# Kernel tuning notes

Hardware: AMD Instinct MI355X
Metric: run time of the kernel (lower is better)

The kernel has to match this reference:

```python
import jax, jax.numpy as jnp
import numpy as np
from jax.nn import gelu

L = 4        # N_layers
M = 32       # N_modes
PA = 48      # n_processor_a
PB = 48      # n_processor_b
P = PA + PB
IN_A, IN_B = 3, 3
OUT_A, OUT_B = 1, 1
HA, HB = 256, 128
K = 3        # kernel_size
S3 = 0.05


def setup_inputs() -> dict:
    key = jax.random.key(0)
    ks = jax.random.split(key, 24)
    n = lambda k, shp, s=1.0: jax.random.normal(k, shp, dtype=jnp.float32) * s
    w_sc = 0.1
    inp = {
        "u_a": n(ks[0], (1, HA, HA)),
        "x_a": n(ks[1], (2, HA, HA)),
        "u_b": n(ks[2], (1, HB, HB)),
        "x_b": n(ks[3], (2, HB, HB)),
        # 1x1 convs stored as (Cout, Cin) matrices (equinox stores (Cout,Cin,1,1); same math)
        "enc_a_w": n(ks[4], (PA, IN_A), w_sc), "enc_a_b": n(ks[5], (PA,), w_sc),
        "enc_b_w": n(ks[6], (PB, IN_B), w_sc), "enc_b_b": n(ks[7], (PB,), w_sc),
        "dec_a_w": n(ks[8], (OUT_A, PA), w_sc), "dec_a_b": n(ks[9], (OUT_A,), w_sc),
        "dec_b_w": n(ks[10], (OUT_B, PB), w_sc), "dec_b_b": n(ks[11], (OUT_B,), w_sc),
        "c1a_w": n(ks[12], (L, PA, PA), w_sc), "c1a_b": n(ks[13], (L, PA), w_sc),
        "c2a_w": n(ks[14], (L, PA, PA), w_sc), "c2a_b": n(ks[15], (L, PA), w_sc),
        "c1b_w": n(ks[16], (L, PB, PB, K, K), w_sc), "c1b_b": n(ks[17], (L, PB), w_sc),
        "c2b_w": n(ks[18], (L, PB, PB, K, K), w_sc), "c2b_b": n(ks[19], (L, PB), w_sc),
        # complex spectral weights A as real/imag float32 parts
        "A_re": n(ks[20], (L, P, P, M, M), S3),
        "A_im": n(ks[21], (L, P, P, M, M), S3),
    }
    return inp


def _conv1x1(x, w, b):
    # x: (Cin, H, W), w: (Cout, Cin)
    return jnp.einsum("oi,ihw->ohw", w, x) + b[:, None, None]


def _convk(x, w, b):
    # x: (Cin, H, W), w: (Cout, Cin, K, K), SAME padding (padding = K//2)
    y = jax.lax.conv_general_dilated(x[None], w, (1, 1), "SAME",
                                     dimension_numbers=("NCHW", "OIHW", "NCHW"))[0]
    return y + b[:, None, None]


def _rfft2_truncate(x, m):
    c = jnp.fft.rfft2(x, norm="forward")[:, :, :m]
    return jnp.roll(c, m // 2, axis=1)[:, :m]


def _irfft2_pad(c, m, s):
    c = jnp.pad(c, ((0, 0), (0, s[0] - c.shape[1]), (0, s[1] - c.shape[2])))
    c = jnp.roll(c, -m // 2, axis=1)
    return jnp.fft.irfft2(c, s=s, norm="forward")


def _spectral(ua, ub, W):
    m = W.shape[2]
    coeff = jnp.concatenate([_rfft2_truncate(ua, m), _rfft2_truncate(ub, m)], axis=0)  # (P, m, m)
    coeff = jnp.einsum("pqmn,qmn->pmn", W, coeff)
    oa = _irfft2_pad(coeff[: ua.shape[0]], m, ua.shape[1:])
    ob = _irfft2_pad(coeff[ua.shape[0]:], m, ub.shape[1:])
    return oa, ob


def reference(u_a, x_a, u_b, x_b,
              enc_a_w, enc_a_b, enc_b_w, enc_b_b,
              dec_a_w, dec_a_b, dec_b_w, dec_b_b,
              c1a_w, c1a_b, c2a_w, c2a_b,
              c1b_w, c1b_b, c2b_w, c2b_b,
              A_re, A_im):
    ua = _conv1x1(jnp.concatenate([x_a, u_a], 0), enc_a_w, enc_a_b)
    ub = _conv1x1(jnp.concatenate([x_b, u_b], 0), enc_b_w, enc_b_b)
    for i in range(A_re.shape[0]):
        Wi = (A_re[i] + 1j * A_im[i]).astype(jnp.complex64)
        ua_, ub_ = _spectral(ua, ub, Wi)
        ua = ua + gelu(_conv1x1(gelu(_conv1x1(ua_, c1a_w[i], c1a_b[i])), c2a_w[i], c2a_b[i]))
        ub = ub + gelu(_convk(gelu(_convk(ub_, c1b_w[i], c1b_b[i])), c2b_w[i], c2b_b[i]))
    out_a = _conv1x1(ua, dec_a_w, dec_a_b)
    out_b = _conv1x1(ub, dec_b_w, dec_b_b)
    return (out_a, out_b)
```

## Files before the change

### kernel.cpp

```cpp
#include <hip/hip_runtime.h>

#define HA 256
#define WA 256
#define HB 128
#define WB 128
#define PA 48
#define PB 48
#define PP 96
#define MM 32
#define NPIXA (HA*WA)
#define NPIXB (HB*WB)

typedef short bf16x8 __attribute__((ext_vector_type(8)));
typedef float f32x4 __attribute__((ext_vector_type(4)));

__device__ __forceinline__ float gelu_f(float x) {
    float z = 0.7978845608028654f * (x + 0.044715f * x * x * x);
    float e = __expf(2.0f * z);
    return x - x / (e + 1.0f);
}

__device__ __forceinline__ short f2bf(float f) {
    unsigned u = __float_as_uint(f);
    unsigned r = (u + 0x7FFFu + ((u >> 16) & 1u)) >> 16;
    return (short)r;
}

__device__ __forceinline__ unsigned pack2(float a, float b) {
    return (unsigned)(unsigned short)f2bf(a) | ((unsigned)(unsigned short)f2bf(b) << 16);
}

__global__ __launch_bounds__(256) void k_pre(
        float* tiyA, float* tixB, float* tiyB, short* T2x,
        const float* u_a, const float* x_a, const float* u_b, const float* x_b,
        const float* wa, const float* ba, const float* wb, const float* bb,
        float* UA, float* UB,
        const float* c1b_w, const float* c2b_w, short* WT,
        short* TbfA, short* TbfB,
        const float* c1a_w, const float* c2a_w, short* WcT,
        short* Ty2A, short* Ty2B,
        short* TyIA, short* TyIB, short* T2xB) {
    const float TWO_PI = 6.28318530717958647692f;
    int bid = blockIdx.x;
    if (bid < 48) {
        int t = bid * 256 + threadIdx.x;
        if (t < MM * WA) {
            int k = t / WA, x = t - k * WA;
            int m = (k * x) & (WA - 1);
            float ang = TWO_PI * (float)m / (float)WA;
            float s, c; __sincosf(ang, &s, &c);
            float wgt = (k == 0) ? 1.0f : 2.0f;
            T2x[x*64 + 2*k]   = f2bf(wgt * c);
            T2x[x*64 + 2*k+1] = f2bf(-wgt * s);
            int ky = k - 16;
            int my = (ky * x) & (HA - 1);
            float angy = TWO_PI * (float)my / (float)HA;
            float sy, cy; __sincosf(angy, &sy, &cy);
            tiyA[2*t] = cy; tiyA[2*t+1] = sy;
        } else if (t < MM * WA + MM * WB) {
            int t2 = t - MM * WA;
            int k = t2 / WB, x = t2 - k * WB;
            int m = (k * x) & (WB - 1);
            float ang = TWO_PI * (float)m / (float)WB;
            float s, c; __sincosf(ang, &s, &c);
            float wgt = (k == 0) ? 1.0f : 2.0f;
            tixB[2*t2] = wgt * c; tixB[2*t2+1] = wgt * s;
            int ky = k - 16;
            int my = (ky * x) & (HB - 1);
            float angy = TWO_PI * (float)my / (float)HB;
            float sy, cy; __sincosf(angy, &sy, &cy);
            tiyB[2*t2] = cy; tiyB[2*t2+1] = sy;
        }
    } else if (bid < 15408) {
        int eb = bid - 48;
        int o = eb / 320;
        int chunk = eb - o * 320;
        if (chunk < 256) {
            int pix = chunk * 256 + threadIdx.x;
            UA[(size_t)o*NPIXA + pix] = wa[o*3+0]*x_a[pix] + wa[o*3+1]*x_a[NPIXA+pix]
                                      + wa[o*3+2]*u_a[pix] + ba[o];
        } else {
            int pix = (chunk - 256) * 256 + threadIdx.x;
            UB[(size_t)o*NPIXB + pix] = wb[o*3+0]*x_b[pix] + wb[o*3+1]*x_b[NPIXB+pix]
                                      + wb[o*3+2]*u_b[pix] + bb[o];
        }
    } else if (bid < 16272) {
        int g = (bid - 15408) * 256 + threadIdx.x;
        if (g < 4*2*9*48*64) {
            int l  = g / 55296;
            int r1 = g - l*55296;
            int cv = r1 / 27648;
            int r2 = r1 - cv*27648;
            int tap = r2 / 3072;
            int r3 = r2 - tap*3072;
            int oc = r3 >> 6;
            int ic = r3 & 63;
            const float* src = cv ? c2b_w : c1b_w;
            float v = 0.f;
            if (ic < 48) v = src[(((size_t)l*48 + oc)*48 + ic)*9 + tap];
            WT[g] = f2bf(v);
        }
    } else if (bid < 16336) {
        int g = (bid - 16272) * 256 + threadIdx.x;
        int col = g >> 8, x = g & 255;
        int k = col >> 1, comp = col & 1;
        int m = (k * x) & (WA - 1);
        float ang = TWO_PI * (float)m / (float)WA;
        float s, c; __sincosf(ang, &s, &c);
        float sc = 1.0f / (float)(HA * WA);
        TbfA[col*WA + x] = f2bf(comp ? -s * sc : c * sc);
    } else if (bid < 16368) {
        int g = (bid - 16336) * 256 + threadIdx.x;
        int col = g >> 7, x = g & 127;
        int k = col >> 1, comp = col & 1;
        int m = (k * x) & (WB - 1);
        float ang = TWO_PI * (float)m / (float)WB;
        float s, c; __sincosf(ang, &s, &c);
        float sc = 1.0f / (float)(HB * WB);
        TbfB[col*WB + x] = f2bf(comp ? -s * sc : c * sc);
    } else if (bid < 16464) {
        int g = (bid - 16368) * 256 + threadIdx.x;
        int l  = g / 6144;
        int r  = g - l*6144;
        int cv = r / 3072;
        int r2 = r - cv*3072;
        int oc = r2 >> 6;
        int ic = r2 & 63;
        const float* src = cv ? c2a_w : c1a_w;
        float v = 0.f;
        if (ic < 48) v = src[((size_t)l*48 + oc)*48 + ic];
        WcT[g] = f2bf(v);
    } else if (bid < 16592) {
        int g = (bid - 16464) * 256 + threadIdx.x;
        int row = g >> 9, col = g & 511;
        int j = row >> 1, comp = row & 1;
        int y = col >> 1, comp2 = col & 1;
        int my = ((j - 16) * y) & (HA - 1);
        float ang = TWO_PI * (float)my / (float)HA;
        float sy, cy; __sincosf(ang, &sy, &cy);
        float v = comp == 0 ? (comp2 == 0 ? cy : sy) : (comp2 == 0 ? -sy : cy);
        Ty2A[g] = f2bf(v);
    } else if (bid < 16656) {
        int g = (bid - 16592) * 256 + threadIdx.x;
        int row = g >> 8, col = g & 255;
        int j = row >> 1, comp = row & 1;
        int y = col >> 1, comp2 = col & 1;
        int my = ((j - 16) * y) & (HB - 1);
        float ang = TWO_PI * (float)my / (float)HB;
        float sy, cy; __sincosf(ang, &sy, &cy);
        float v = comp == 0 ? (comp2 == 0 ? cy : sy) : (comp2 == 0 ? -sy : cy);
        Ty2B[g] = f2bf(v);
    } else if (bid < 16720) {
        int g = (bid - 16656) * 256 + threadIdx.x;
        int y = g >> 6, col = g & 63;
        int j = col >> 1, comp = col & 1;
        int my = ((j - 16) * y) & (HA - 1);
        float ang = TWO_PI * (float)my / (float)HA;
        float sy, cy; __sincosf(ang, &sy, &cy);
        TyIA[g] = f2bf(comp ? sy : cy);
    } else if (bid < 16752) {
        int g = (bid - 16720) * 256 + threadIdx.x;
        int y = g >> 6, col = g & 63;
        int j = col >> 1, comp = col & 1;
        int my = ((j - 16) * y) & (HB - 1);
        float ang = TWO_PI * (float)my / (float)HB;
        float sy, cy; __sincosf(ang, &sy, &cy);
        TyIB[g] = f2bf(comp ? sy : cy);
    } else {
        int g = (bid - 16752) * 256 + threadIdx.x;
        int x = g >> 6, col = g & 63;
        int k = col >> 1, comp = col & 1;
        int m = (k * x) & (WB - 1);
        float ang = TWO_PI * (float)m / (float)WB;
        float s, c; __sincosf(ang, &s, &c);
        float wgt = (k == 0) ? 1.0f : 2.0f;
        T2xB[g] = f2bf(comp ? -wgt * s : wgt * c);
    }
}

__global__ __launch_bounds__(256) void k_fwd_x(
        const float* __restrict__ UA, const float* __restrict__ UB,
        short* __restrict__ FTA, short* __restrict__ FTB,
        const short* __restrict__ TbfA, const short* __restrict__ TbfB) {
    extern __shared__ short lsb[];
    int bid = blockIdx.x;
    const float* U; short* FT; const short* T; int N, ymask, cshift;
    if (bid < 384) { U = UA; FT = FTA; T = TbfA; N = WA; ymask = 255; cshift = 8; }
    else { bid -= 384; U = UB; FT = FTB; T = TbfB; N = WB; ymask = 127; cshift = 7; }
    int r0 = bid * 32;
    int c = r0 >> cshift;
    int ybase = r0 & ymask;
    int NP = N + 8;
    int nq = N >> 2;
    const float4* src = (const float4*)(U + (size_t)r0 * N);
    for (int i = threadIdx.x; i < 32*nq; i += 256) {
        int r = i / nq, q = i - r*nq;
        float4 v = src[i];
        *(uint2*)(lsb + r*NP + q*4) = make_uint2(pack2(v.x, v.y), pack2(v.z, v.w));
    }
    __syncthreads();
    int wv = threadIdx.x >> 6, lane = threadIdx.x & 63;
    int n = lane & 15, kg = lane >> 4;
    int col = wv*16 + n;
    const short* Tc = T + (size_t)col * N;
    f32x4 acc0 = {0.f,0.f,0.f,0.f}, acc1 = {0.f,0.f,0.f,0.f};
    for (int ks = 0; ks < (N >> 5); ++ks) {
        bf16x8 bfrag = *(const bf16x8*)(Tc + ks*32 + kg*8);
        bf16x8 a0 = *(const bf16x8*)(lsb + (size_t)n*NP + ks*32 + kg*8);
        bf16x8 a1 = *(const bf16x8*)(lsb + (size_t)(16+n)*NP + ks*32 + kg*8);
        acc0 = __builtin_amdgcn_mfma_f32_16x16x32_bf16(a0, bfrag, acc0, 0, 0, 0);
        acc1 = __builtin_amdgcn_mfma_f32_16x16x32_bf16(a1, bfrag, acc1, 0, 0, 0);
    }
    __syncthreads();
    short* trb = lsb;
    #pragma unroll
    for (int r = 0; r < 4; ++r) {
        trb[col*36 + kg*4 + r]      = f2bf(acc0[r]);
        trb[col*36 + 16 + kg*4 + r] = f2bf(acc1[r]);
    }
    __syncthreads();
    int K2 = 2 * (ymask + 1);
    for (int idx = threadIdx.x; idx < 512; idx += 256) {
        int kx = idx >> 4, q = idx & 15;
        int yl = q * 2;
        unsigned lo = (unsigned)(unsigned short)trb[(2*kx+0)*36 + yl]
                    | ((unsigned)(unsigned short)trb[(2*kx+1)*36 + yl] << 16);
        unsigned hi = (unsigned)(unsigned short)trb[(2*kx+0)*36 + yl+1]
                    | ((unsigned)(unsigned short)trb[(2*kx+1)*36 + yl+1] << 16);
        *(uint2*)(FT + ((size_t)(c*32 + kx))*K2 + 2*(size_t)ybase + yl*2) = make_uint2(lo, hi);
    }
}

__global__ __launch_bounds__(256) void k_fwd_y(
        const short* __restrict__ FTA, const short* __restrict__ FTB,
        const short* __restrict__ Ty2A, const short* __restrict__ Ty2B,
        float* __restrict__ CINa, float* __restrict__ CINb) {
    __shared__ short lsb[32*264];
    int bid = blockIdx.x;
    const short* FT; const short* Ty; int K2, NP, pbase, c, h;
    if (bid < 96) { c = bid>>1; h = bid&1; FT = FTA; Ty = Ty2A; K2 = 512; NP = 264; pbase = 0; }
    else { int b2 = bid - 96; c = b2>>1; h = b2&1; FT = FTB; Ty = Ty2B; K2 = 256; NP = 136; pbase = 48; }
    float* CO = (h == 0) ? CINa : CINb;
    int hlen = K2 >> 1;
    int nchunk = hlen >> 3;
    for (int idx = threadIdx.x; idx < 32*nchunk; idx += 256) {
        int row = idx / nchunk, q = idx - row*nchunk;
        *(uint4*)(lsb + row*NP + q*8) =
            *(const uint4*)(FT + ((size_t)c*32 + row)*K2 + h*hlen + q*8);
    }
    __syncthreads();
    int w = threadIdx.x >> 6, lane = threadIdx.x & 63;
    int n = lane & 15, kg = lane >> 4;
    f32x4 acc0 = {0.f,0.f,0.f,0.f}, acc1 = {0.f,0.f,0.f,0.f};
    int nks = hlen >> 5;
    for (int ks = 0; ks < nks; ++ks) {
        bf16x8 af = *(const bf16x8*)(Ty + (size_t)(w*16 + n)*K2 + h*hlen + ks*32 + kg*8);
        bf16x8 b0 = *(const bf16x8*)(lsb + n*NP + ks*32 + kg*8);
        bf16x8 b1 = *(const bf16x8*)(lsb + (16+n)*NP + ks*32 + kg*8);
        acc0 = __builtin_amdgcn_mfma_f32_16x16x32_bf16(af, b0, acc0, 0, 0, 0);
        acc1 = __builtin_amdgcn_mfma_f32_16x16x32_bf16(af, b1, acc1, 0, 0, 0);
    }
    #pragma unroll
    for (int r = 0; r < 4; ++r) {
        int row = w*16 + kg*4 + r;
        int j = row >> 1, comp = row & 1;
        size_t base = (((size_t)(pbase + c))*32 + j)*32;
        CO[(base + n)*2 + comp]      = acc0[r];
        CO[(base + 16 + n)*2 + comp] = acc1[r];
    }
}

__global__ __launch_bounds__(256) void k_spectral(
        const float* __restrict__ Wre, const float* __restrict__ Wim,
        const float* __restrict__ CINa, const float* __restrict__ CINb,
        float2* __restrict__ PART) {
    int part = blockIdx.y;
    int t = blockIdx.x * 256 + threadIdx.x;
    int p = t >> 8;
    int m4 = (t & 255) << 2;
    int q0 = part * 12;
    const float4* wr = (const float4*)(Wre + ((size_t)p * PP + q0) * 1024 + m4);
    const float4* wi = (const float4*)(Wim + ((size_t)p * PP + q0) * 1024 + m4);
    const float4* ca = (const float4*)(CINa + (size_t)q0 * 2048 + m4*2);
    const float4* cb = (const float4*)(CINb + (size_t)q0 * 2048 + m4*2);
    float re0=0,re1=0,re2=0,re3=0, im0=0,im1=0,im2=0,im3=0;
    #pragma unroll
    for (int q = 0; q < 12; ++q) {
        float4 a = wr[q * 256];
        float4 b = wi[q * 256];
        float4 c0 = ca[q * 512];
        float4 c1 = ca[q * 512 + 1];
        float4 d0 = cb[q * 512];
        float4 d1 = cb[q * 512 + 1];
        float cr0 = c0.x + d0.x, ci0 = c0.y + d0.y;
        float cr1 = c0.z + d0.z, ci1 = c0.w + d0.w;
        float cr2 = c1.x + d1.x, ci2 = c1.y + d1.y;
        float cr3 = c1.z + d1.z, ci3 = c1.w + d1.w;
        re0 += a.x*cr0 - b.x*ci0;  im0 += a.x*ci0 + b.x*cr0;
        re1 += a.y*cr1 - b.y*ci1;  im1 += a.y*ci1 + b.y*cr1;
        re2 += a.z*cr2 - b.z*ci2;  im2 += a.z*ci2 + b.z*cr2;
        re3 += a.w*cr3 - b.w*ci3;  im3 += a.w*ci3 + b.w*cr3;
    }
    float2* po = PART + ((size_t)part * PP + p) * 1024 + m4;
    po[0] = make_float2(re0, im0);
    po[1] = make_float2(re1, im1);
    po[2] = make_float2(re2, im2);
    po[3] = make_float2(re3, im3);
}

__global__ __launch_bounds__(256) void k_invy(
        const float2* __restrict__ PART,
        const short* __restrict__ TyIA, const short* __restrict__ TyIB,
        short* __restrict__ DA, short* __restrict__ DB) {
    __shared__ short A2[64*72];
    int bid = blockIdx.x;
    int c, yh, cb; const short* Ty; short* D;
    if (bid < 96) { c = bid >> 1; yh = bid & 1; Ty = TyIA; D = DA; cb = c; }
    else { c = bid - 96 + 48; yh = 0; Ty = TyIB; D = DB; cb = c - 48; }
    for (int idx = threadIdx.x; idx < 1024; idx += 256) {
        int j = idx >> 5, kx = idx & 31;
        float re = 0.f, im = 0.f;
        const float2* pp = PART + (size_t)c*1024 + idx;
        #pragma unroll
        for (int u = 0; u < 8; ++u) {
            float2 v = pp[(size_t)u*PP*1024];
            re += v.x; im += v.y;
        }
        A2[(2*kx+0)*72 + 2*j]   = f2bf(re);
        A2[(2*kx+0)*72 + 2*j+1] = f2bf(-im);
        A2[(2*kx+1)*72 + 2*j]   = f2bf(im);
        A2[(2*kx+1)*72 + 2*j+1] = f2bf(re);
    }
    __syncthreads();
    int wv = threadIdx.x >> 6, lane = threadIdx.x & 63;
    int n = lane & 15, kg = lane >> 4;
    #pragma unroll
    for (int ntl = 0; ntl < 2; ++ntl) {
        int nt = wv*2 + ntl;
        int y = yh*128 + nt*16 + n;
        bf16x8 bf0 = *(const bf16x8*)(Ty + (size_t)y*64 + kg*8);
        bf16x8 bf1 = *(const bf16x8*)(Ty + (size_t)y*64 + 32 + kg*8);
        #pragma unroll
        for (int mt = 0; mt < 4; ++mt) {
            bf16x8 a0 = *(const bf16x8*)(A2 + (mt*16 + n)*72 + kg*8);
            bf16x8 a1 = *(const bf16x8*)(A2 + (mt*16 + n)*72 + 32 + kg*8);
            f32x4 acc = {0.f,0.f,0.f,0.f};
            acc = __builtin_amdgcn_mfma_f32_16x16x32_bf16(a0, bf0, acc, 0, 0, 0);
            acc = __builtin_amdgcn_mfma_f32_16x16x32_bf16(a1, bf1, acc, 0, 0, 0);
            int row0 = mt*16 + kg*4;
            *(uint2*)(D + (size_t)y*3072 + cb*64 + row0) =
                make_uint2(pack2(acc[0], acc[1]), pack2(acc[2], acc[3]));
        }
    }
}

__global__ __launch_bounds__(256) void k_inv(
        const short* __restrict__ DA, const short* __restrict__ DB,
        float* __restrict__ UA, short* __restrict__ SBbf,
        const short* __restrict__ T2x, const short* __restrict__ T2xB,
        const short* __restrict__ W1T, const short* __restrict__ W2T,
        const float* __restrict__ b1v, const float* __restrict__ b2v) {
    __shared__ __attribute__((aligned(16))) char smc[37888];
    int t = threadIdx.x;
    int wv = t >> 6, lane = t & 63;
    int n = lane & 15, kg = lane >> 4;
    if (blockIdx.x < 512) {
        short* b0bf  = (short*)smc;
        short* slbf  = (short*)(smc + 18432);
        float* bl1   = (float*)(smc + 37120);
        float* bl2   = (float*)(smc + 37312);
        int y  = blockIdx.x >> 1;
        int xh = (blockIdx.x & 1) << 7;
        if (t >= 64 && t < 112) bl1[t-64] = b1v[t-64];
        if (t >= 128 && t < 176) bl2[t-128] = b2v[t-128];
        const short* DAy = DA + (size_t)y*3072;
        {
            f32x4 acc[2][3];
            #pragma unroll
            for (int i = 0; i < 2; ++i)
                #pragma unroll
                for (int mt = 0; mt < 3; ++mt)
                    acc[i][mt] = (f32x4){0.f,0.f,0.f,0.f};
            #pragma unroll
            for (int ks = 0; ks < 2; ++ks) {
                bf16x8 bfr[2];
                #pragma unroll
                for (int i = 0; i < 2; ++i) {
                    int px = xh + (wv*2 + i)*16 + n;
                    bfr[i] = *(const bf16x8*)(T2x + (size_t)px*64 + ks*32 + kg*8);
                }
                #pragma unroll
                for (int mt = 0; mt < 3; ++mt) {
                    bf16x8 af = *(const bf16x8*)(DAy + (mt*16 + n)*64 + ks*32 + kg*8);
                    #pragma unroll
                    for (int i = 0; i < 2; ++i)
                        acc[i][mt] = __builtin_amdgcn_mfma_f32_16x16x32_bf16(af, bfr[i], acc[i][mt], 0, 0, 0);
                }
            }
            #pragma unroll
            for (int i = 0; i < 2; ++i) {
                int xl = (wv*2 + i)*16 + n;
                #pragma unroll
                for (int mt = 0; mt < 3; ++mt)
                    #pragma unroll
                    for (int r = 0; r < 4; ++r)
                        slbf[xl*72 + mt*16 + kg*4 + r] = f2bf(acc[i][mt][r]);
            }
            for (int idx = t; idx < 2048; idx += 256)
                slbf[(idx >> 4)*72 + 48 + (idx & 15)] = 0;
        }
        __syncthreads();
        {
            bf16x8 aw[3][2];
            #pragma unroll
            for (int mt = 0; mt < 3; ++mt)
                #pragma unroll
                for (int ks = 0; ks < 2; ++ks)
                    aw[mt][ks] = *(const bf16x8*)(W1T + (size_t)(mt*16 + n)*64 + ks*32 + kg*8);
            f32x4 acc[2][3];
            #pragma unroll
            for (int nt = 0; nt < 2; ++nt)
                #pragma unroll
                for (int mt = 0; mt < 3; ++mt)
                    acc[nt][mt] = (f32x4){0.f,0.f,0.f,0.f};
            #pragma unroll
            for (int nt = 0; nt < 2; ++nt) {
                int ntile = wv*2 + nt;
                #pragma unroll
                for (int ks = 0; ks < 2; ++ks) {
                    bf16x8 bfrag = *(const bf16x8*)(slbf + (size_t)(ntile*16 + n)*72 + ks*32 + kg*8);
                    #pragma unroll
                    for (int mt = 0; mt < 3; ++mt)
                        acc[nt][mt] = __builtin_amdgcn_mfma_f32_16x16x32_bf16(aw[mt][ks], bfrag, acc[nt][mt], 0, 0, 0);
                }
            }
            #pragma unroll
            for (int nt = 0; nt < 2; ++nt) {
                int px = (wv*2 + nt)*16 + n;
                #pragma unroll
                for (int mt = 0; mt < 3; ++mt) {
                    int oc0 = mt*16 + kg*4;
                    float g0 = gelu_f(acc[nt][mt][0] + bl1[oc0+0]);
                    float g1 = gelu_f(acc[nt][mt][1] + bl1[oc0+1]);
                    float g2 = gelu_f(acc[nt][mt][2] + bl1[oc0+2]);
                    float g3 = gelu_f(acc[nt][mt][3] + bl1[oc0+3]);
                    *(uint2*)(b0bf + (size_t)px*72 + oc0) = make_uint2(pack2(g0,g1), pack2(g2,g3));
                }
            }
            for (int idx = t; idx < 2048; idx += 256)
                b0bf[(idx >> 4)*72 + 48 + (idx & 15)] = 0;
        }
        __syncthreads();
        {
            bf16x8 aw[3][2];
            #pragma unroll
            for (int mt = 0; mt < 3; ++mt)
                #pragma unroll
                for (int ks = 0; ks < 2; ++ks)
                    aw[mt][ks] = *(const bf16x8*)(W2T + (size_t)(mt*16 + n)*64 + ks*32 + kg*8);
            f32x4 acc[2][3];
            #pragma unroll
            for (int nt = 0; nt < 2; ++nt)
                #pragma unroll
                for (int mt = 0; mt < 3; ++mt)
                    acc[nt][mt] = (f32x4){0.f,0.f,0.f,0.f};
            #pragma unroll
            for (int nt = 0; nt < 2; ++nt) {
                int ntile = wv*2 + nt;
                #pragma unroll
                for (int ks = 0; ks < 2; ++ks) {
                    bf16x8 bfrag = *(const bf16x8*)(b0bf + (size_t)(ntile*16 + n)*72 + ks*32 + kg*8);
                    #pragma unroll
                    for (int mt = 0; mt < 3; ++mt)
                        acc[nt][mt] = __builtin_amdgcn_mfma_f32_16x16x32_bf16(aw[mt][ks], bfrag, acc[nt][mt], 0, 0, 0);
                }
            }
            #pragma unroll
            for (int nt = 0; nt < 2; ++nt) {
                int px = (wv*2 + nt)*16 + n;
                #pragma unroll
                for (int mt = 0; mt < 3; ++mt) {
                    int oc0 = mt*16 + kg*4;
                    #pragma unroll
                    for (int r = 0; r < 4; ++r) {
                        int oc = oc0 + r;
                        size_t o = (size_t)oc*NPIXA + (size_t)y*WA + xh + px;
                        UA[o] = gelu_f(acc[nt][mt][r] + bl2[oc]) + UA[o];
                    }
                }
            }
        }
    } else {
        int y = blockIdx.x - 512;
        short* sbuf = (short*)smc;
        const short* DBy = DB + (size_t)y*3072;
        #pragma unroll
        for (int ntl = 0; ntl < 2; ++ntl) {
            int nt = wv*2 + ntl;
            int x = nt*16 + n;
            bf16x8 bf0 = *(const bf16x8*)(T2xB + (size_t)x*64 + kg*8);
            bf16x8 bf1 = *(const bf16x8*)(T2xB + (size_t)x*64 + 32 + kg*8);
            #pragma unroll
            for (int mt = 0; mt < 3; ++mt) {
                bf16x8 a0 = *(const bf16x8*)(DBy + (mt*16 + n)*64 + kg*8);
                bf16x8 a1 = *(const bf16x8*)(DBy + (mt*16 + n)*64 + 32 + kg*8);
                f32x4 acc = {0.f,0.f,0.f,0.f};
                acc = __builtin_amdgcn_mfma_f32_16x16x32_bf16(a0, bf0, acc, 0, 0, 0);
                acc = __builtin_amdgcn_mfma_f32_16x16x32_bf16(a1, bf1, acc, 0, 0, 0);
                int c0 = mt*16 + kg*4;
                #pragma unroll
                for (int r = 0; r < 4; ++r)
                    sbuf[(c0 + r)*132 + x] = f2bf(acc[r]);
            }
        }
        __syncthreads();
        for (int idx = t; idx < 768; idx += 256) {
            int cc = idx >> 4, q = idx & 15;
            uint4 v = *(const uint4*)(sbuf + cc*132 + q*8);
            *(uint4*)(SBbf + (size_t)cc*NPIXB + (size_t)y*WB + q*8) = v;
        }
    }
}

__global__ __launch_bounds__(256) void k_conv3x3_mfma(
        const short* __restrict__ in, float* __restrict__ outf,
        short* __restrict__ outbf,
        const short* __restrict__ wt, const float* __restrict__ bias,
        const float* resid) {
    __shared__ float smf[3072];
    short* tile = (short*)smf;
    int y  = blockIdx.x >> 3;
    int x0 = (blockIdx.x & 7) << 4;
    int tid = threadIdx.x;

    for (int idx = tid; idx < 3456; idx += 256) {
        int r = idx / 1152;
        int rem = idx - r*1152;
        int ic = rem / 18;
        int px = rem - ic*18;
        int gy = y - 1 + r, gx = x0 - 1 + px;
        short v = 0;
        if (ic < 48 && gy >= 0 && gy < HB && gx >= 0 && gx < WB)
            v = in[(size_t)ic*NPIXB + gy*WB + gx];
        tile[(r*18 + px)*72 + ic] = v;
    }
    __syncthreads();

    int w = tid >> 6, lane = tid & 63;
    int n = lane & 15, kg = lane >> 4, m = lane & 15;
    f32x4 acc0 = {0.f,0.f,0.f,0.f}, acc1 = {0.f,0.f,0.f,0.f}, acc2 = {0.f,0.f,0.f,0.f};
    for (int s = w; s < 18; s += 4) {
        int tap = s >> 1;
        int kb = (s & 1) << 5;
        int dy = tap / 3, dx = tap - dy*3;
        bf16x8 bfrag = *(const bf16x8*)(tile + ((dy*18 + n + dx)*72 + kb + kg*8));
        const short* ap = wt + ((size_t)tap*48)*64 + kb + kg*8;
        bf16x8 a0 = *(const bf16x8*)(ap + (size_t)(m     )*64);
        bf16x8 a1 = *(const bf16x8*)(ap + (size_t)(16 + m)*64);
        bf16x8 a2 = *(const bf16x8*)(ap + (size_t)(32 + m)*64);
        acc0 = __builtin_amdgcn_mfma_f32_16x16x32_bf16(a0, bfrag, acc0, 0, 0, 0);
        acc1 = __builtin_amdgcn_mfma_f32_16x16x32_bf16(a1, bfrag, acc1, 0, 0, 0);
        acc2 = __builtin_amdgcn_mfma_f32_16x16x32_bf16(a2, bfrag, acc2, 0, 0, 0);
    }
    __syncthreads();
    float4* red = (float4*)smf;
    red[(w*3 + 0)*64 + lane] = make_float4(acc0[0], acc0[1], acc0[2], acc0[3]);
    red[(w*3 + 1)*64 + lane] = make_float4(acc1[0], acc1[1], acc1[2], acc1[3]);
    red[(w*3 + 2)*64 + lane] = make_float4(acc2[0], acc2[1], acc2[2], acc2[3]);
    __syncthreads();
    if (tid < 192) {
        int mt = tid >> 6, ln = tid & 63;
        float4 s0 = red[(0*3 + mt)*64 + ln];
        float4 s1 = red[(1*3 + mt)*64 + ln];
        float4 s2 = red[(2*3 + mt)*64 + ln];
        float4 s3 = red[(3*3 + mt)*64 + ln];
        float sum[4];
        sum[0] = s0.x + s1.x + s2.x + s3.x;
        sum[1] = s0.y + s1.y + s2.y + s3.y;
        sum[2] = s0.z + s1.z + s2.z + s3.z;
        sum[3] = s0.w + s1.w + s2.w + s3.w;
        int px = x0 + (ln & 15);
        #pragma unroll
        for (int r = 0; r < 4; ++r) {
            int oc = mt*16 + (ln >> 4)*4 + r;
            float v = sum[r] + bias[oc];
            v = gelu_f(v);
            size_t o = (size_t)oc*NPIXB + (size_t)y*WB + px;
            if (outbf) {
                outbf[o] = f2bf(v);
            } else {
                if (resid) v += resid[o];
                outf[o] = v;
            }
        }
    }
}

__global__ __launch_bounds__(256) void k_decode(
        const float* __restrict__ UA, const float* __restrict__ UB,
        const float* dwa, const float* dba,
        const float* dwb, const float* dbb, float* outp) {
    int t = blockIdx.x*256 + threadIdx.x;
    if (t < NPIXA) {
        float acc = dba[0];
        #pragma unroll 8
        for (int p = 0; p < PA; ++p) acc += dwa[p]*UA[(size_t)p*NPIXA + t];
        outp[t] = acc;
    } else {
        int u = t - NPIXA;
        float acc = dbb[0];
        #pragma unroll 8
        for (int p = 0; p < PB; ++p) acc += dwb[p]*UB[(size_t)p*NPIXB + u];
        outp[t] = acc;
    }
}

extern "C" void kernel_launch(void* const* d_in, const int* in_sizes, int n_in,
                              void* d_out, int out_size, void* d_ws, size_t ws_size,
                              hipStream_t stream) {
    const float* u_a   = (const float*)d_in[0];
    const float* x_a   = (const float*)d_in[1];
    const float* u_b   = (const float*)d_in[2];
    const float* x_b   = (const float*)d_in[3];
    const float* enc_a_w = (const float*)d_in[4];
    const float* enc_a_b = (const float*)d_in[5];
    const float* enc_b_w = (const float*)d_in[6];
    const float* enc_b_b = (const float*)d_in[7];
    const float* dec_a_w = (const float*)d_in[8];
    const float* dec_a_b = (const float*)d_in[9];
    const float* dec_b_w = (const float*)d_in[10];
    const float* dec_b_b = (const float*)d_in[11];
    const float* c1a_w = (const float*)d_in[12];
    const float* c1a_b = (const float*)d_in[13];
    const float* c2a_w = (const float*)d_in[14];
    const float* c2a_b = (const float*)d_in[15];
    const float* c1b_w = (const float*)d_in[16];
    const float* c1b_b = (const float*)d_in[17];
    const float* c2b_w = (const float*)d_in[18];
    const float* c2b_b = (const float*)d_in[19];
    const float* A_re = (const float*)d_in[20];
    const float* A_im = (const float*)d_in[21];

    float* ws = (float*)d_ws;
    size_t off = 0;
    auto alloc = [&](size_t n) { float* p = ws + off; off += n; return p; };
    short* WT    = (short*)alloc(4*2*9*48*64/2);
    short* TbfA  = (short*)alloc(64*WA/2);
    short* TbfB  = (short*)alloc(64*WB/2);
    short* WcT   = (short*)alloc(4*2*48*64/2);
    short* T2x   = (short*)alloc(WA*64/2);
    short* T2xB  = (short*)alloc(WB*64/2);
    short* Ty2A  = (short*)alloc(64*512/2);
    short* Ty2B  = (short*)alloc(64*256/2);
    short* TyIA  = (short*)alloc(HA*64/2);
    short* TyIB  = (short*)alloc(HB*64/2);
    float* TiyA  = alloc(MM*HA*2);
    float* TixB  = alloc(MM*WB*2);
    float* TiyB  = alloc(MM*HB*2);
    float* UA = alloc((size_t)PA*NPIXA);
    float* UB = alloc((size_t)PB*NPIXB);
    short* SBbf = (short*)alloc((size_t)PB*NPIXB/2);
    short* TBbf = (short*)alloc((size_t)PB*NPIXB/2);
    short* FTA = (short*)alloc((size_t)PA*MM*512/2);
    short* FTB = (short*)alloc((size_t)PB*MM*256/2);
    short* DA  = (short*)alloc((size_t)HA*3072/2);
    short* DB  = (short*)alloc((size_t)HB*3072/2);
    float* CINa = alloc((size_t)PP*MM*MM*2);
    float* CINb = alloc((size_t)PP*MM*MM*2);
    float2* PART = (float2*)alloc((size_t)8*PP*MM*MM*2);
    if (off * sizeof(float) > ws_size) return;

    k_pre<<<dim3(16784), dim3(256), 0, stream>>>(
        TiyA, TixB, TiyB, T2x,
        u_a,x_a,u_b,x_b, enc_a_w,enc_a_b,enc_b_w,enc_b_b, UA,UB,
        c1b_w, c2b_w, WT, TbfA, TbfB, c1a_w, c2a_w, WcT, Ty2A, Ty2B,
        TyIA, TyIB, T2xB);
    for (int l = 0; l < 4; ++l) {
        k_fwd_x<<<dim3(576), dim3(256), 32*(WA+8)*2, stream>>>(UA,UB,FTA,FTB,TbfA,TbfB);
        k_fwd_y<<<dim3(192), dim3(256), 0, stream>>>(FTA,FTB,Ty2A,Ty2B,CINa,CINb);
        k_spectral<<<dim3(96,8), dim3(256), 0, stream>>>(
            A_re + (size_t)l*PP*PP*MM*MM, A_im + (size_t)l*PP*PP*MM*MM,
            CINa, CINb, PART);
        k_invy<<<dim3(144), dim3(256), 0, stream>>>(PART, TyIA, TyIB, DA, DB);
        k_inv<<<dim3(512 + 128), dim3(256), 0, stream>>>(DA, DB, UA, SBbf,
            T2x, T2xB,
            WcT + (size_t)(l*2 + 0)*3072, WcT + (size_t)(l*2 + 1)*3072,
            c1a_b + (size_t)l*PA, c2a_b + (size_t)l*PA);
        k_conv3x3_mfma<<<dim3(1024), dim3(256), 0, stream>>>(SBbf, (float*)nullptr, TBbf,
            WT + (size_t)(l*2 + 0)*27648, c1b_b + (size_t)l*PB, (const float*)nullptr);
        k_conv3x3_mfma<<<dim3(1024), dim3(256), 0, stream>>>(TBbf, UB, (short*)nullptr,
            WT + (size_t)(l*2 + 1)*27648, c2b_b + (size_t)l*PB, UB);
    }
    k_decode<<<dim3(320), dim3(256), 0, stream>>>(UA, UB,
        dec_a_w, dec_a_b, dec_b_w, dec_b_b, (float*)d_out);
}
```

Before: 341.0 us.

## Switch branch-B bf16 activations to pixel-major layout and restructure 3x3 conv MFMA

The bf16 intermediates for the branch-B 3x3 convolutions are now stored pixel-major (48 channels contiguous per pixel) rather than channel-major. The conv kernel can then load its halo tile with 16-byte vector loads instead of scalar gathers. The conv kernel now covers 32 pixels per block with 6 waves, each owning one 16x16 output tile across all taps. This removes the cross-wave shared-memory reduction and its extra barriers, and the first conv writes packed bf16 pairs. In exchange the block and grid shapes change, and the channel-major fp32 output stores keep a strided pattern.

Measured after the change: 308.0 us (median of 2 runs). 1.11x faster.

```diff
diff --git a/kernel.cpp b/kernel.cpp
--- a/kernel.cpp
+++ b/kernel.cpp
@@ -514,84 +514,71 @@
             }
         }
         __syncthreads();
-        for (int idx = t; idx < 768; idx += 256) {
-            int cc = idx >> 4, q = idx & 15;
-            uint4 v = *(const uint4*)(sbuf + cc*132 + q*8);
-            *(uint4*)(SBbf + (size_t)cc*NPIXB + (size_t)y*WB + q*8) = v;
-        }
-    }
-}
-
-__global__ __launch_bounds__(256) void k_conv3x3_mfma(
+        for (int idx = t; idx < 3072; idx += 256) {
+            int x = idx / 24, cu = idx - x*24;
+            unsigned v = (unsigned)(unsigned short)sbuf[(2*cu)*132 + x]
+                       | ((unsigned)(unsigned short)sbuf[(2*cu+1)*132 + x] << 16);
+            *(unsigned*)(SBbf + ((size_t)y*WB + x)*48 + 2*cu) = v;
+        }
+    }
+}
+
+__global__ __launch_bounds__(384) void k_conv3x3_mfma(
         const short* __restrict__ in, float* __restrict__ outf,
         short* __restrict__ outbf,
         const short* __restrict__ wt, const float* __restrict__ bias,
         const float* resid) {
-    __shared__ float smf[3072];
-    short* tile = (short*)smf;
-    int y  = blockIdx.x >> 3;
-    int x0 = (blockIdx.x & 7) << 4;
+    __shared__ __attribute__((aligned(16))) short tile[3*34*72];
+    int y  = blockIdx.x >> 2;
+    int x0 = (blockIdx.x & 3) << 5;
     int tid = threadIdx.x;
-
-    for (int idx = tid; idx < 3456; idx += 256) {
-        int r = idx / 1152;
-        int rem = idx - r*1152;
-        int ic = rem / 18;
-        int px = rem - ic*18;
+    for (int idx = tid; idx < 102*6; idx += 384) {
+        int pix = idx / 6, chunk = idx - pix*6;
+        int r = pix / 34, px = pix - r*34;
         int gy = y - 1 + r, gx = x0 - 1 + px;
-        short v = 0;
-        if (ic < 48 && gy >= 0 && gy < HB && gx >= 0 && gx < WB)
-            v = in[(size_t)ic*NPIXB + gy*WB + gx];
-        tile[(r*18 + px)*72 + ic] = v;
+        uint4 v = {0u,0u,0u,0u};
+        if (gy >= 0 && gy < HB && gx >= 0 && gx < WB)
+            v = *(const uint4*)(in + ((size_t)gy*WB + gx)*48 + chunk*8);
+        *(uint4*)(tile + pix*72 + chunk*8) = v;
+    }
+    for (int idx = tid; idx < 102*2; idx += 384) {
+        int pix = idx >> 1, h = idx & 1;
+        *(uint4*)(tile + pix*72 + 48 + h*8) = (uint4){0u,0u,0u,0u};
     }
     __syncthreads();
 
-    int w = tid >> 6, lane = tid & 63;
-    int n = lane & 15, kg = lane >> 4, m = lane & 15;
-    f32x4 acc0 = {0.f,0.f,0.f,0.f}, acc1 = {0.f,0.f,0.f,0.f}, acc2 = {0.f,0.f,0.f,0.f};
-    for (int s = w; s < 18; s += 4) {
-        int tap = s >> 1;
-        int kb = (s & 1) << 5;
+    int wv = tid / 64, lane = tid & 63;
+    int n = lane & 15, kg = lane >> 4;
+    int nt = wv & 1, mt = wv >> 1;
+    f32x4 acc = {0.f,0.f,0.f,0.f};
+    #pragma unroll
+    for (int tap = 0; tap < 9; ++tap) {
         int dy = tap / 3, dx = tap - dy*3;
-        bf16x8 bfrag = *(const bf16x8*)(tile + ((dy*18 + n + dx)*72 + kb + kg*8));
-        const short* ap = wt + ((size_t)tap*48)*64 + kb + kg*8;
-        bf16x8 a0 = *(const bf16x8*)(ap + (size_t)(m     )*64);
-        bf16x8 a1 = *(const bf16x8*)(ap + (size_t)(16 + m)*64);
-        bf16x8 a2 = *(const bf16x8*)(ap + (size_t)(32 + m)*64);
-        acc0 = __builtin_amdgcn_mfma_f32_16x16x32_bf16(a0, bfrag, acc0, 0, 0, 0);
-        acc1 = __builtin_amdgcn_mfma_f32_16x16x32_bf16(a1, bfrag, acc1, 0, 0, 0);
-        acc2 = __builtin_amdgcn_mfma_f32_16x16x32_bf16(a2, bfrag, acc2, 0, 0, 0);
-    }
-    __syncthreads();
-    float4* red = (float4*)smf;
-    red[(w*3 + 0)*64 + lane] = make_float4(acc0[0], acc0[1], acc0[2], acc0[3]);
-    red[(w*3 + 1)*64 + lane] = make_float4(acc1[0], acc1[1], acc1[2], acc1[3]);
-    red[(w*3 + 2)*64 + lane] = make_float4(acc2[0], acc2[1], acc2[2], acc2[3]);
-    __syncthreads();
-    if (tid < 192) {
-        int mt = tid >> 6, ln = tid & 63;
-        float4 s0 = red[(0*3 + mt)*64 + ln];
-        float4 s1 = red[(1*3 + mt)*64 + ln];
-        float4 s2 = red[(2*3 + mt)*64 + ln];
-        float4 s3 = red[(3*3 + mt)*64 + ln];
-        float sum[4];
-        sum[0] = s0.x + s1.x + s2.x + s3.x;
-        sum[1] = s0.y + s1.y + s2.y + s3.y;
-        sum[2] = s0.z + s1.z + s2.z + s3.z;
-        sum[3] = s0.w + s1.w + s2.w + s3.w;
-        int px = x0 + (ln & 15);
+        int pxl = nt*16 + n + dx;
+        const short* brow = tile + (dy*34 + pxl)*72;
+        const short* ap = wt + (size_t)tap*3072 + (size_t)(mt*16 + n)*64;
+        #pragma unroll
+        for (int ks = 0; ks < 2; ++ks) {
+            bf16x8 bfrag = *(const bf16x8*)(brow + ks*32 + kg*8);
+            bf16x8 afrag = *(const bf16x8*)(ap + ks*32 + kg*8);
+            acc = __builtin_amdgcn_mfma_f32_16x16x32_bf16(afrag, bfrag, acc, 0, 0, 0);
+        }
+    }
+    int px_g = x0 + nt*16 + n;
+    int oc0 = mt*16 + kg*4;
+    float g0 = gelu_f(acc[0] + bias[oc0+0]);
+    float g1 = gelu_f(acc[1] + bias[oc0+1]);
+    float g2 = gelu_f(acc[2] + bias[oc0+2]);
+    float g3 = gelu_f(acc[3] + bias[oc0+3]);
+    if (outbf) {
+        *(uint2*)(outbf + ((size_t)y*WB + px_g)*48 + oc0) =
+            make_uint2(pack2(g0, g1), pack2(g2, g3));
+    } else {
+        float gv[4] = {g0, g1, g2, g3};
         #pragma unroll
         for (int r = 0; r < 4; ++r) {
-            int oc = mt*16 + (ln >> 4)*4 + r;
-            float v = sum[r] + bias[oc];
-            v = gelu_f(v);
-            size_t o = (size_t)oc*NPIXB + (size_t)y*WB + px;
-            if (outbf) {
-                outbf[o] = f2bf(v);
-            } else {
-                if (resid) v += resid[o];
-                outf[o] = v;
-            }
+            size_t o = (size_t)(oc0 + r)*NPIXB + (size_t)y*WB + px_g;
+            outf[o] = gv[r] + resid[o];
         }
     }
 }
@@ -686,9 +673,9 @@
             T2x, T2xB,
             WcT + (size_t)(l*2 + 0)*3072, WcT + (size_t)(l*2 + 1)*3072,
             c1a_b + (size_t)l*PA, c2a_b + (size_t)l*PA);
-        k_conv3x3_mfma<<<dim3(1024), dim3(256), 0, stream>>>(SBbf, (float*)nullptr, TBbf,
+        k_conv3x3_mfma<<<dim3(512), dim3(384), 0, stream>>>(SBbf, (float*)nullptr, TBbf,
             WT + (size_t)(l*2 + 0)*27648, c1b_b + (size_t)l*PB, (const float*)nullptr);
-        k_conv3x3_mfma<<<dim3(1024), dim3(256), 0, stream>>>(TBbf, UB, (short*)nullptr,
+        k_conv3x3_mfma<<<dim3(512), dim3(384), 0, stream>>>(TBbf, UB, (short*)nullptr,
             WT + (size_t)(l*2 + 1)*27648, c2b_b + (size_t)l*PB, UB);
     }
     k_decode<<<dim3(320), dim3(256), 0, stream>>>(UA, UB,
```
